# Kernel optimization log

Hardware: AMD Instinct MI355X
Metric: run time of the kernel (lower is better)

Reference implementation:

```python
import jax, jax.numpy as jnp
import numpy as np

B, L, DIM = 1, 2048, 512
DHEAD = 64
HEADS = DIM // DHEAD  # 8
KS = 127              # kernel_size (odd)
EXP = 4


def setup_inputs() -> dict:
    key = jax.random.key(0)
    ks = jax.random.split(key, 8)
    sc = 0.02
    rnd = lambda k, shape: (jax.random.normal(k, shape, jnp.float32) * sc)
    return {
        "x": jax.random.normal(ks[0], (B, L, DIM), jnp.float32),
        "ln1_g": jnp.ones((DIM,), jnp.float32),
        "ln1_b": jnp.zeros((DIM,), jnp.float32),
        "qkv_w": rnd(ks[1], (DIM, 3 * DIM)),
        "qkv_b": jnp.zeros((3 * DIM,), jnp.float32),
        "rpb": rnd(ks[2], (HEADS, 2 * KS - 1)),
        "proj_w": rnd(ks[3], (DIM, DIM)),
        "proj_b": jnp.zeros((DIM,), jnp.float32),
        "ln2_g": jnp.ones((DIM,), jnp.float32),
        "ln2_b": jnp.zeros((DIM,), jnp.float32),
        "ff1_w": rnd(ks[4], (DIM, DIM * EXP)),
        "ff1_b": jnp.zeros((DIM * EXP,), jnp.float32),
        "ff2_w": rnd(ks[5], (DIM * EXP, DIM)),
        "ff2_b": jnp.zeros((DIM,), jnp.float32),
    }


def _layernorm(x, g, b, eps=1e-5):
    m = x.mean(-1, keepdims=True)
    v = ((x - m) ** 2).mean(-1, keepdims=True)
    return (x - m) * jax.lax.rsqrt(v + eps) * g + b


def _neighborhood_attn_1d(x, qkv_w, qkv_b, rpb, proj_w, proj_b):
    # NATTEN NeighborhoodAttention1D: window of KS keys per query, clamped
    # at sequence edges so every query sees exactly KS keys (requires L >= KS).
    b, l, dim = x.shape
    qkv = (x @ qkv_w + qkv_b).reshape(b, l, 3, HEADS, DHEAD)
    q, k, v = qkv[:, :, 0], qkv[:, :, 1], qkv[:, :, 2]  # [b,l,h,d]
    scale = DHEAD ** -0.5
    # window start per query, clamped to stay in-bounds
    starts = jnp.clip(jnp.arange(l) - KS // 2, 0, l - KS)          # [l]
    idx = starts[:, None] + jnp.arange(KS)                         # [l,KS]
    kg = k[:, idx]                                                 # [b,l,KS,h,d]
    vg = v[:, idx]                                                 # [b,l,KS,h,d]
    logits = jnp.einsum('blhd,blkhd->blhk', q * scale, kg)         # [b,l,h,KS]
    # relative-position bias: index = (j - i) + (KS - 1), in [0, 2KS-2]
    bias_idx = idx - jnp.arange(l)[:, None] + (KS - 1)             # [l,KS]
    logits = logits + rpb[:, bias_idx].transpose(1, 0, 2)[None]    # [1,l,h,KS]
    attn = jax.nn.softmax(logits, axis=-1)
    out = jnp.einsum('blhk,blkhd->blhd', attn, vg).reshape(b, l, dim)
    return out @ proj_w + proj_b


def reference(x, ln1_g, ln1_b, qkv_w, qkv_b, rpb, proj_w, proj_b,
              ln2_g, ln2_b, ff1_w, ff1_b, ff2_w, ff2_b):
    x = x + _neighborhood_attn_1d(_layernorm(x, ln1_g, ln1_b),
                                  qkv_w, qkv_b, rpb, proj_w, proj_b)
    h = _layernorm(x, ln2_g, ln2_b)
    h = jax.nn.gelu(h @ ff1_w + ff1_b, approximate=False) @ ff2_w + ff2_b
    return x + h
```

## Files before the change

kernel.cpp:

```cpp
#include <hip/hip_runtime.h>
#include <hip/hip_bf16.h>

static constexpr int Lc     = 2048;
static constexpr int DIMc   = 512;
static constexpr int HEADSc = 8;
static constexpr int DHEADc = 64;
static constexpr int KSc    = 127;
static constexpr int NQKVc  = 1536;

typedef __attribute__((ext_vector_type(8))) short short8;
typedef __attribute__((ext_vector_type(4))) float f32x4;
typedef unsigned short u16;
typedef unsigned int u32;

__device__ __forceinline__ float b2f(u16 s) {
  return __uint_as_float(((u32)s) << 16);
}
__device__ __forceinline__ u16 f2b(float x) {
  u32 u = __float_as_uint(x);
  return (u16)((u + 0x7fffu + ((u >> 16) & 1u)) >> 16);
}
__device__ __forceinline__ void gload16(const void* g, void* l) {
  __builtin_amdgcn_global_load_lds(
      (const __attribute__((address_space(1))) u32*)g,
      (__attribute__((address_space(3))) u32*)l, 16, 0, 0);
}

__global__ __launch_bounds__(256) void prep_kernel(
    const float* __restrict__ w0, const float* __restrict__ w1,
    const float* __restrict__ w2, const float* __restrict__ w3,
    u16* __restrict__ o0, u16* __restrict__ o1, u16* __restrict__ o2,
    u16* __restrict__ o3, const float* __restrict__ xin,
    const float* __restrict__ g, const float* __restrict__ b,
    u16* __restrict__ lnout) {
  __shared__ float tl[32][33];
  __shared__ float rs[4], rq[4], stat[2];
  const int tid = threadIdx.x;
  if (blockIdx.x >= 3072) {
    const int row = blockIdx.x - 3072;
    const float* rp = xin + (size_t)row * DIMc;
    float v0 = rp[tid];
    float v1 = rp[tid + 256];
    float s = v0 + v1;
    float sq = v0 * v0 + v1 * v1;
#pragma unroll
    for (int o = 32; o > 0; o >>= 1) {
      s += __shfl_down(s, o);
      sq += __shfl_down(sq, o);
    }
    const int wid = tid >> 6, lane = tid & 63;
    if (lane == 0) { rs[wid] = s; rq[wid] = sq; }
    __syncthreads();
    if (tid == 0) {
      float S = rs[0] + rs[1] + rs[2] + rs[3];
      float Q = rq[0] + rq[1] + rq[2] + rq[3];
      float m = S / DIMc;
      float var = Q / DIMc - m * m;
      stat[0] = m;
      stat[1] = rsqrtf(var + 1e-5f);
    }
    __syncthreads();
    const float m = stat[0], r = stat[1];
    lnout[(size_t)row * DIMc + tid] = f2b((v0 - m) * r * g[tid] + b[tid]);
    lnout[(size_t)row * DIMc + tid + 256] =
        f2b((v1 - m) * r * g[tid + 256] + b[tid + 256]);
    return;
  }
  int t = blockIdx.x;
  const float* W;
  u16* O;
  int K, N;
  if (t < 768)       { W = w0; O = o0; K = 512;  N = 1536; }
  else if (t < 1024) { W = w1; O = o1; K = 512;  N = 512;  t -= 768; }
  else if (t < 2048) { W = w2; O = o2; K = 512;  N = 2048; t -= 1024; }
  else               { W = w3; O = o3; K = 2048; N = 512;  t -= 2048; }
  const int nt = N >> 5;
  const int by = t / nt, bx = t % nt;
  const int c4 = tid & 7, r = tid >> 3;
  {
    const f32x4 v =
        *(const f32x4*)(W + (size_t)(by * 32 + r) * N + bx * 32 + c4 * 4);
    tl[r][c4 * 4 + 0] = v[0];
    tl[r][c4 * 4 + 1] = v[1];
    tl[r][c4 * 4 + 2] = v[2];
    tl[r][c4 * 4 + 3] = v[3];
  }
  __syncthreads();
  {
    ushort4 pk = {f2b(tl[c4 * 4 + 0][r]), f2b(tl[c4 * 4 + 1][r]),
                  f2b(tl[c4 * 4 + 2][r]), f2b(tl[c4 * 4 + 3][r])};
    *(ushort4*)(O + (size_t)(bx * 32 + r) * K + by * 32 + c4 * 4) = pk;
  }
}

__global__ __launch_bounds__(256) void ln2_kernel(const float* __restrict__ in,
                                                  const float* __restrict__ g,
                                                  const float* __restrict__ b,
                                                  u16* __restrict__ out) {
  const int row = blockIdx.x;
  const int tid = threadIdx.x;
  const float* rp = in + (size_t)row * DIMc;
  float v0 = rp[tid];
  float v1 = rp[tid + 256];
  float s = v0 + v1;
  float sq = v0 * v0 + v1 * v1;
  __shared__ float rs[4], rq[4], stat[2];
#pragma unroll
  for (int o = 32; o > 0; o >>= 1) {
    s += __shfl_down(s, o);
    sq += __shfl_down(sq, o);
  }
  const int wid = tid >> 6, lane = tid & 63;
  if (lane == 0) { rs[wid] = s; rq[wid] = sq; }
  __syncthreads();
  if (tid == 0) {
    float S = rs[0] + rs[1] + rs[2] + rs[3];
    float Q = rq[0] + rq[1] + rq[2] + rq[3];
    float m = S / DIMc;
    float var = Q / DIMc - m * m;
    stat[0] = m;
    stat[1] = rsqrtf(var + 1e-5f);
  }
  __syncthreads();
  const float m = stat[0], r = stat[1];
  out[(size_t)row * DIMc + tid] = f2b((v0 - m) * r * g[tid] + b[tid]);
  out[(size_t)row * DIMc + tid + 256] =
      f2b((v1 - m) * r * g[tid + 256] + b[tid + 256]);
}

template <int OP, typename OUT_T>
__global__ __launch_bounds__(128) void mfma_gemm(
    const u16* __restrict__ A, const u16* __restrict__ Bt,
    const float* __restrict__ bias, const float* __restrict__ res,
    OUT_T* __restrict__ C, int M, int N, int K) {
  constexpr int BK = 64;
  __shared__ __align__(16) u16 As[2][64 * BK];
  __shared__ __align__(16) u16 Bs[2][64 * BK];
  const int tid = threadIdx.x;
  const int wave = tid >> 6, lane = tid & 63;
  const int m0 = blockIdx.y * 64, n0 = blockIdx.x * 64;
  const int wn = wave * 32;
  const int T = K / BK;

  f32x4 acc[4][2] = {};

  const int fr = lane & 15;
  const int hi = lane >> 4;

  const int lrow = wave * 8 + (lane >> 3);
  const int lcol = ((lane & 7) ^ (lane >> 3)) * 8;

#define STAGE(k0, buf)                                                        \
  {                                                                           \
    _Pragma("unroll") for (int p = 0; p < 4; ++p) {                           \
      gload16(A + (size_t)(m0 + p * 16 + lrow) * K + (k0) + lcol,             \
              &As[buf][p * 1024 + wave * 512]);                               \
      gload16(Bt + (size_t)(n0 + p * 16 + lrow) * K + (k0) + lcol,            \
              &Bs[buf][p * 1024 + wave * 512]);                               \
    }                                                                         \
  }

  STAGE(0, 0);
  STAGE(BK, 1);

  for (int t = 0; t < T; ++t) {
    const int cur = t & 1;
    if (t + 1 < T) {
      asm volatile("s_waitcnt vmcnt(8)" ::: "memory");
    } else {
      asm volatile("s_waitcnt vmcnt(0)" ::: "memory");
    }
    __builtin_amdgcn_s_barrier();

    short8 af[4][2], bf[2][2];
#pragma unroll
    for (int i = 0; i < 4; ++i) {
      const int row = i * 16 + fr;
      const char* rb = (const char*)As[cur] + row * 128;
#pragma unroll
      for (int ks = 0; ks < 2; ++ks)
        af[i][ks] =
            *(const short8*)(rb + ((ks * 64 + hi * 16) ^ ((fr & 7) << 4)));
    }
#pragma unroll
    for (int j = 0; j < 2; ++j) {
      const int row = wn + j * 16 + fr;
      const char* rb = (const char*)Bs[cur] + row * 128;
#pragma unroll
      for (int ks = 0; ks < 2; ++ks)
        bf[j][ks] =
            *(const short8*)(rb + ((ks * 64 + hi * 16) ^ ((fr & 7) << 4)));
    }
    asm volatile("s_waitcnt lgkmcnt(0)" ::: "memory");
    __builtin_amdgcn_sched_barrier(0);
    __builtin_amdgcn_s_barrier();

    if (t + 2 < T) STAGE((t + 2) * BK, cur);

#pragma unroll
    for (int ks = 0; ks < 2; ++ks)
#pragma unroll
      for (int i = 0; i < 4; ++i)
#pragma unroll
        for (int j = 0; j < 2; ++j)
          acc[i][j] = __builtin_amdgcn_mfma_f32_16x16x32_bf16(
              af[i][ks], bf[j][ks], acc[i][j], 0, 0, 0);
  }
#undef STAGE

  const int cl = lane & 15;
  const int rbase = (lane >> 4) * 4;
#pragma unroll
  for (int i = 0; i < 4; ++i) {
#pragma unroll
    for (int j = 0; j < 2; ++j) {
      const int c = n0 + wn + j * 16 + cl;
      const float bv = bias[c];
#pragma unroll
      for (int r = 0; r < 4; ++r) {
        const int row = m0 + i * 16 + rbase + r;
        float v = acc[i][j][r] + bv;
        if (OP == 1) v = 0.5f * v * (1.0f + erff(v * 0.70710678118f));
        ((u16*)C)[(size_t)row * N + c] = f2b(v);
      }
    }
  }
}

__global__ __launch_bounds__(256, 1) void mfma_gemm_ks(
    const u16* __restrict__ A, const u16* __restrict__ Bt,
    const float* __restrict__ bias, const float* __restrict__ res,
    float* __restrict__ C, int M, int N, int K) {
  constexpr int BK = 32;
  __shared__ __align__(16) char LB[65536];
  const int tid = threadIdx.x;
  const int wave = tid >> 6, lane = tid & 63;
  const int m0 = blockIdx.y * 64, n0 = blockIdx.x * 64;
  const int kslice = K >> 2;
  const int kbeg = wave * kslice;
  const int T = kslice / BK;
  char* myb = LB + wave * 16384;

  f32x4 acc[4][4] = {};
  const int fr = lane & 15;
  const int hi = lane >> 4;

  const int lrow = lane >> 2;
  const int lcol = ((lane & 3) ^ ((lane >> 2) & 3)) * 8;

#define KSTAGE(k0, b)                                                         \
  {                                                                           \
    _Pragma("unroll") for (int p = 0; p < 4; ++p) {                           \
      gload16(A + (size_t)(m0 + p * 16 + lrow) * K + (k0) + lcol,             \
              myb + (b) * 8192 + p * 1024);                                   \
      gload16(Bt + (size_t)(n0 + p * 16 + lrow) * K + (k0) + lcol,            \
              myb + (b) * 8192 + 4096 + p * 1024);                            \
    }                                                                         \
  }

  KSTAGE(kbeg, 0);
  KSTAGE(kbeg + BK, 1);

  for (int t = 0; t < T; ++t) {
    const int cur = t & 1;
    if (t + 1 < T) {
      asm volatile("s_waitcnt vmcnt(8)" ::: "memory");
    } else {
      asm volatile("s_waitcnt vmcnt(0)" ::: "memory");
    }

    short8 af[4], bf[4];
#pragma unroll
    for (int i = 0; i < 4; ++i) {
      const char* rb = myb + cur * 8192 + (i * 16 + fr) * 64;
      af[i] = *(const short8*)(rb + ((hi * 16) ^ ((fr & 3) << 4)));
    }
#pragma unroll
    for (int j = 0; j < 4; ++j) {
      const char* rb = myb + cur * 8192 + 4096 + (j * 16 + fr) * 64;
      bf[j] = *(const short8*)(rb + ((hi * 16) ^ ((fr & 3) << 4)));
    }
    asm volatile("s_waitcnt lgkmcnt(0)" ::: "memory");
    __builtin_amdgcn_sched_barrier(0);

    if (t + 2 < T) KSTAGE(kbeg + (t + 2) * BK, cur);

    __builtin_amdgcn_s_setprio(1);
#pragma unroll
    for (int i = 0; i < 4; ++i)
#pragma unroll
      for (int j = 0; j < 4; ++j)
        acc[i][j] = __builtin_amdgcn_mfma_f32_16x16x32_bf16(af[i], bf[j],
                                                            acc[i][j], 0, 0, 0);
    __builtin_amdgcn_s_setprio(0);
  }
#undef KSTAGE

  __syncthreads();
  float* red = (float*)LB;
  const int rbase = hi * 4;
#pragma unroll
  for (int i = 0; i < 4; ++i)
#pragma unroll
    for (int j = 0; j < 4; ++j)
#pragma unroll
      for (int r = 0; r < 4; ++r)
        red[wave * 4096 + (i * 16 + rbase + r) * 64 + j * 16 + fr] =
            acc[i][j][r];
  __syncthreads();
#pragma unroll
  for (int q = 0; q < 4; ++q) {
    const int idx = q * 1024 + tid * 4;
    const int row = idx >> 6, col = idx & 63;
    f32x4 s = *(const f32x4*)&red[idx];
#pragma unroll
    for (int w = 1; w < 4; ++w) s += *(const f32x4*)&red[w * 4096 + idx];
    const f32x4 bb = *(const f32x4*)&bias[n0 + col];
    const size_t o = (size_t)(m0 + row) * N + n0 + col;
    const f32x4 rr = *(const f32x4*)&res[o];
    s += bb + rr;
    *(f32x4*)&C[o] = s;
  }
}

__global__ __launch_bounds__(256) void attn_mfma(const u16* __restrict__ qkv,
                                                 const float* __restrict__ rpb,
                                                 u16* __restrict__ out) {
  constexpr int NR = 192, NT = 12, PP = 200;
  __shared__ __align__(16) u16 Ks[NR * DHEADc];
  __shared__ __align__(16) u16 Vt[DHEADc * NR];
  __shared__ __align__(16) u16 Ps[4][16 * PP];
  __shared__ float rp[2 * KSc - 1];
  const int h = blockIdx.y, l0 = blockIdx.x * 64, tid = threadIdx.x;
  const int wv = tid >> 6, lane = tid & 63;
  const int fr = lane & 15, hi = lane >> 4;

  int s_min = l0 - 63;
  if (s_min < 0) s_min = 0;
  if (s_min > Lc - KSc) s_min = Lc - KSc;

  for (int i = tid; i < 2 * KSc - 1; i += 256) rp[i] = rpb[h * (2 * KSc - 1) + i];

#pragma unroll
  for (int rd = 0; rd < 6; ++rd) {
    const int linear = rd * 4096 + wv * 1024 + lane * 16;
    const int row = linear >> 7;
    const int seg = (linear >> 4) & 7;
    const int segp = seg ^ (row & 7);
    int gl = s_min + row;
    if (gl > Lc - 1) gl = Lc - 1;
    gload16(qkv + (size_t)gl * NQKVc + DIMc + h * DHEADc + segp * 8,
            (char*)Ks + rd * 4096 + wv * 1024);
  }

#pragma unroll
  for (int rd = 0; rd < 3; ++rd) {
    const int t = rd * 256 + tid;
    const int rpair = t >> 3, seg = t & 7;
    const int r0 = rpair * 2;
    int g0 = s_min + r0, g1 = s_min + r0 + 1;
    if (g0 > Lc - 1) g0 = Lc - 1;
    if (g1 > Lc - 1) g1 = Lc - 1;
    const short8 a =
        *(const short8*)(qkv + (size_t)g0 * NQKVc + 2 * DIMc + h * DHEADc + seg * 8);
    const short8 bq =
        *(const short8*)(qkv + (size_t)g1 * NQKVc + 2 * DIMc + h * DHEADc + seg * 8);
#pragma unroll
    for (int j = 0; j < 8; ++j) {
      const int d = seg * 8 + j;
      int byte = d * (NR * 2) + r0 * 2;
      byte ^= (d & 7) << 4;
      *(u32*)((char*)Vt + byte) =
          ((u32)(u16)a[j]) | (((u32)(u16)bq[j]) << 16);
    }
  }

  const int lq = l0 + wv * 16 + fr;
  short8 qf[2];
#pragma unroll
  for (int ks = 0; ks < 2; ++ks)
    qf[ks] = *(const short8*)(qkv + (size_t)lq * NQKVc + h * DHEADc + ks * 32 + hi * 8);

  __syncthreads();

  f32x4 S[NT] = {};
  __builtin_amdgcn_s_setprio(1);
#pragma unroll
  for (int jt = 0; jt < NT; ++jt) {
#pragma unroll
    for (int ks = 0; ks < 2; ++ks) {
      int byte = (jt * 16 + fr) * 128 + ks * 64 + hi * 16;
      byte ^= (fr & 7) << 4;
      const short8 kf = *(const short8*)((const char*)Ks + byte);
      S[jt] = __builtin_amdgcn_mfma_f32_16x16x32_bf16(qf[ks], kf, S[jt], 0, 0, 0);
    }
  }
  __builtin_amdgcn_s_setprio(0);

  float inv4[4];
#pragma unroll
  for (int r = 0; r < 4; ++r) {
    const int l = l0 + wv * 16 + hi * 4 + r;
    int st = l - 63;
    if (st < 0) st = 0;
    if (st > Lc - KSc) st = Lc - KSc;
    float mx = -3e38f;
#pragma unroll
    for (int jt = 0; jt < NT; ++jt) {
      const int pos = s_min + jt * 16 + fr;
      const int j = pos - st;
      float v = -3e38f;
      if (j >= 0 && j <= KSc - 1) v = S[jt][r] * 0.125f + rp[pos - l + KSc - 1];
      S[jt][r] = v;
      mx = fmaxf(mx, v);
    }
#pragma unroll
    for (int o = 1; o < 16; o <<= 1) mx = fmaxf(mx, __shfl_xor(mx, o));
    float sum = 0.f;
#pragma unroll
    for (int jt = 0; jt < NT; ++jt) {
      const float e = __expf(S[jt][r] - mx);
      S[jt][r] = e;
      sum += e;
    }
#pragma unroll
    for (int o = 1; o < 16; o <<= 1) sum += __shfl_xor(sum, o);
    inv4[r] = 1.f / sum;
  }

#pragma unroll
  for (int jt = 0; jt < NT; ++jt)
#pragma unroll
    for (int r = 0; r < 4; ++r)
      Ps[wv][(hi * 4 + r) * PP + jt * 16 + fr] = f2b(S[jt][r] * inv4[r]);

  f32x4 O[4] = {};
  __builtin_amdgcn_s_setprio(1);
#pragma unroll
  for (int ks = 0; ks < 6; ++ks) {
    const short8 pa =
        *(const short8*)((const char*)Ps[wv] + fr * (PP * 2) + ks * 64 + hi * 16);
#pragma unroll
    for (int dt = 0; dt < 4; ++dt) {
      int byte = (dt * 16 + fr) * (NR * 2) + ks * 64 + hi * 16;
      byte ^= (fr & 7) << 4;
      const short8 vb = *(const short8*)((const char*)Vt + byte);
      O[dt] = __builtin_amdgcn_mfma_f32_16x16x32_bf16(pa, vb, O[dt], 0, 0, 0);
    }
  }
  __builtin_amdgcn_s_setprio(0);

#pragma unroll
  for (int dt = 0; dt < 4; ++dt)
#pragma unroll
    for (int r = 0; r < 4; ++r)
      out[(size_t)(l0 + wv * 16 + hi * 4 + r) * DIMc + h * DHEADc + dt * 16 + fr] =
          f2b(O[dt][r]);
}

extern "C" void kernel_launch(void* const* d_in, const int* in_sizes, int n_in,
                              void* d_out, int out_size, void* d_ws,
                              size_t ws_size, hipStream_t stream) {
  const float* x      = (const float*)d_in[0];
  const float* ln1_g  = (const float*)d_in[1];
  const float* ln1_b  = (const float*)d_in[2];
  const float* qkv_w  = (const float*)d_in[3];
  const float* qkv_b  = (const float*)d_in[4];
  const float* rpb    = (const float*)d_in[5];
  const float* proj_w = (const float*)d_in[6];
  const float* proj_b = (const float*)d_in[7];
  const float* ln2_g  = (const float*)d_in[8];
  const float* ln2_b  = (const float*)d_in[9];
  const float* ff1_w  = (const float*)d_in[10];
  const float* ff1_b  = (const float*)d_in[11];
  const float* ff2_w  = (const float*)d_in[12];
  const float* ff2_b  = (const float*)d_in[13];
  float* out = (float*)d_out;

  char* ws = (char*)d_ws;
  u16*   lnbuf   = (u16*)(ws);
  u16*   qkvbuf  = (u16*)(ws + ((size_t)2  << 20));
  u16*   attnbuf = (u16*)(ws + ((size_t)8  << 20));
  float* x2      = (float*)(ws + ((size_t)10 << 20));
  u16*   ff1buf  = (u16*)(ws + ((size_t)14 << 20));
  u16*   wt_qkv  = (u16*)(ws + ((size_t)22 << 20));
  u16*   wt_proj = (u16*)(ws + ((size_t)23 << 20) + ((size_t)512 << 10));
  u16*   wt_ff1  = (u16*)(ws + ((size_t)24 << 20));
  u16*   wt_ff2  = (u16*)(ws + ((size_t)26 << 20));

  prep_kernel<<<5120, 256, 0, stream>>>(qkv_w, proj_w, ff1_w, ff2_w, wt_qkv,
                                        wt_proj, wt_ff1, wt_ff2, x, ln1_g,
                                        ln1_b, lnbuf);
  mfma_gemm<0, u16><<<dim3(NQKVc / 64, Lc / 64), 128, 0, stream>>>(
      lnbuf, wt_qkv, qkv_b, nullptr, qkvbuf, Lc, NQKVc, DIMc);
  attn_mfma<<<dim3(Lc / 64, HEADSc), 256, 0, stream>>>(qkvbuf, rpb, attnbuf);
  mfma_gemm_ks<<<dim3(DIMc / 64, Lc / 64), 256, 0, stream>>>(
      attnbuf, wt_proj, proj_b, x, x2, Lc, DIMc, DIMc);
  ln2_kernel<<<Lc, 256, 0, stream>>>(x2, ln2_g, ln2_b, lnbuf);
  mfma_gemm<1, u16><<<dim3(4 * DIMc / 64, Lc / 64), 128, 0, stream>>>(
      lnbuf, wt_ff1, ff1_b, nullptr, ff1buf, Lc, 4 * DIMc, DIMc);
  mfma_gemm_ks<<<dim3(DIMc / 64, Lc / 64), 256, 0, stream>>>(
      ff1buf, wt_ff2, ff2_b, x2, out, Lc, DIMc, 4 * DIMc);
}
```

Before: 67.15 us.

## Fuse proj, LN2, FF1 and FF2 into one persistent kernel with grid barriers

```diff
diff --git a/kernel.cpp b/kernel.cpp
--- a/kernel.cpp
+++ b/kernel.cpp
@@ -32,10 +32,11 @@
     u16* __restrict__ o0, u16* __restrict__ o1, u16* __restrict__ o2,
     u16* __restrict__ o3, const float* __restrict__ xin,
     const float* __restrict__ g, const float* __restrict__ b,
-    u16* __restrict__ lnout) {
+    u16* __restrict__ lnout, u32* __restrict__ bar) {
   __shared__ float tl[32][33];
   __shared__ float rs[4], rq[4], stat[2];
   const int tid = threadIdx.x;
+  if (blockIdx.x == 0 && tid < 8) bar[tid] = 0;
   if (blockIdx.x >= 3072) {
     const int row = blockIdx.x - 3072;
     const float* rp = xin + (size_t)row * DIMc;
@@ -93,46 +94,10 @@
   }
 }
 
-__global__ __launch_bounds__(256) void ln2_kernel(const float* __restrict__ in,
-                                                  const float* __restrict__ g,
-                                                  const float* __restrict__ b,
-                                                  u16* __restrict__ out) {
-  const int row = blockIdx.x;
-  const int tid = threadIdx.x;
-  const float* rp = in + (size_t)row * DIMc;
-  float v0 = rp[tid];
-  float v1 = rp[tid + 256];
-  float s = v0 + v1;
-  float sq = v0 * v0 + v1 * v1;
-  __shared__ float rs[4], rq[4], stat[2];
-#pragma unroll
-  for (int o = 32; o > 0; o >>= 1) {
-    s += __shfl_down(s, o);
-    sq += __shfl_down(sq, o);
-  }
-  const int wid = tid >> 6, lane = tid & 63;
-  if (lane == 0) { rs[wid] = s; rq[wid] = sq; }
-  __syncthreads();
-  if (tid == 0) {
-    float S = rs[0] + rs[1] + rs[2] + rs[3];
-    float Q = rq[0] + rq[1] + rq[2] + rq[3];
-    float m = S / DIMc;
-    float var = Q / DIMc - m * m;
-    stat[0] = m;
-    stat[1] = rsqrtf(var + 1e-5f);
-  }
-  __syncthreads();
-  const float m = stat[0], r = stat[1];
-  out[(size_t)row * DIMc + tid] = f2b((v0 - m) * r * g[tid] + b[tid]);
-  out[(size_t)row * DIMc + tid + 256] =
-      f2b((v1 - m) * r * g[tid + 256] + b[tid + 256]);
-}
-
-template <int OP, typename OUT_T>
 __global__ __launch_bounds__(128) void mfma_gemm(
     const u16* __restrict__ A, const u16* __restrict__ Bt,
-    const float* __restrict__ bias, const float* __restrict__ res,
-    OUT_T* __restrict__ C, int M, int N, int K) {
+    const float* __restrict__ bias, u16* __restrict__ C, int M, int N,
+    int K) {
   constexpr int BK = 64;
   __shared__ __align__(16) u16 As[2][64 * BK];
   __shared__ __align__(16) u16 Bs[2][64 * BK];
@@ -143,10 +108,8 @@
   const int T = K / BK;
 
   f32x4 acc[4][2] = {};
-
   const int fr = lane & 15;
   const int hi = lane >> 4;
-
   const int lrow = wave * 8 + (lane >> 3);
   const int lcol = ((lane & 7) ^ (lane >> 3)) * 8;
 
@@ -219,107 +182,9 @@
 #pragma unroll
       for (int r = 0; r < 4; ++r) {
         const int row = m0 + i * 16 + rbase + r;
-        float v = acc[i][j][r] + bv;
-        if (OP == 1) v = 0.5f * v * (1.0f + erff(v * 0.70710678118f));
-        ((u16*)C)[(size_t)row * N + c] = f2b(v);
+        C[(size_t)row * N + c] = f2b(acc[i][j][r] + bv);
       }
     }
-  }
-}
-
-__global__ __launch_bounds__(256, 1) void mfma_gemm_ks(
-    const u16* __restrict__ A, const u16* __restrict__ Bt,
-    const float* __restrict__ bias, const float* __restrict__ res,
-    float* __restrict__ C, int M, int N, int K) {
-  constexpr int BK = 32;
-  __shared__ __align__(16) char LB[65536];
-  const int tid = threadIdx.x;
-  const int wave = tid >> 6, lane = tid & 63;
-  const int m0 = blockIdx.y * 64, n0 = blockIdx.x * 64;
-  const int kslice = K >> 2;
-  const int kbeg = wave * kslice;
-  const int T = kslice / BK;
-  char* myb = LB + wave * 16384;
-
-  f32x4 acc[4][4] = {};
-  const int fr = lane & 15;
-  const int hi = lane >> 4;
-
-  const int lrow = lane >> 2;
-  const int lcol = ((lane & 3) ^ ((lane >> 2) & 3)) * 8;
-
-#define KSTAGE(k0, b)                                                         \
-  {                                                                           \
-    _Pragma("unroll") for (int p = 0; p < 4; ++p) {                           \
-      gload16(A + (size_t)(m0 + p * 16 + lrow) * K + (k0) + lcol,             \
-              myb + (b) * 8192 + p * 1024);                                   \
-      gload16(Bt + (size_t)(n0 + p * 16 + lrow) * K + (k0) + lcol,            \
-              myb + (b) * 8192 + 4096 + p * 1024);                            \
-    }                                                                         \
-  }
-
-  KSTAGE(kbeg, 0);
-  KSTAGE(kbeg + BK, 1);
-
-  for (int t = 0; t < T; ++t) {
-    const int cur = t & 1;
-    if (t + 1 < T) {
-      asm volatile("s_waitcnt vmcnt(8)" ::: "memory");
-    } else {
-      asm volatile("s_waitcnt vmcnt(0)" ::: "memory");
-    }
-
-    short8 af[4], bf[4];
-#pragma unroll
-    for (int i = 0; i < 4; ++i) {
-      const char* rb = myb + cur * 8192 + (i * 16 + fr) * 64;
-      af[i] = *(const short8*)(rb + ((hi * 16) ^ ((fr & 3) << 4)));
-    }
-#pragma unroll
-    for (int j = 0; j < 4; ++j) {
-      const char* rb = myb + cur * 8192 + 4096 + (j * 16 + fr) * 64;
-      bf[j] = *(const short8*)(rb + ((hi * 16) ^ ((fr & 3) << 4)));
-    }
-    asm volatile("s_waitcnt lgkmcnt(0)" ::: "memory");
-    __builtin_amdgcn_sched_barrier(0);
-
-    if (t + 2 < T) KSTAGE(kbeg + (t + 2) * BK, cur);
-
-    __builtin_amdgcn_s_setprio(1);
-#pragma unroll
-    for (int i = 0; i < 4; ++i)
-#pragma unroll
-      for (int j = 0; j < 4; ++j)
-        acc[i][j] = __builtin_amdgcn_mfma_f32_16x16x32_bf16(af[i], bf[j],
-                                                            acc[i][j], 0, 0, 0);
-    __builtin_amdgcn_s_setprio(0);
-  }
-#undef KSTAGE
-
-  __syncthreads();
-  float* red = (float*)LB;
-  const int rbase = hi * 4;
-#pragma unroll
-  for (int i = 0; i < 4; ++i)
-#pragma unroll
-    for (int j = 0; j < 4; ++j)
-#pragma unroll
-      for (int r = 0; r < 4; ++r)
-        red[wave * 4096 + (i * 16 + rbase + r) * 64 + j * 16 + fr] =
-            acc[i][j][r];
-  __syncthreads();
-#pragma unroll
-  for (int q = 0; q < 4; ++q) {
-    const int idx = q * 1024 + tid * 4;
-    const int row = idx >> 6, col = idx & 63;
-    f32x4 s = *(const f32x4*)&red[idx];
-#pragma unroll
-    for (int w = 1; w < 4; ++w) s += *(const f32x4*)&red[w * 4096 + idx];
-    const f32x4 bb = *(const f32x4*)&bias[n0 + col];
-    const size_t o = (size_t)(m0 + row) * N + n0 + col;
-    const f32x4 rr = *(const f32x4*)&res[o];
-    s += bb + rr;
-    *(f32x4*)&C[o] = s;
   }
 }
 
@@ -456,6 +321,250 @@
     for (int r = 0; r < 4; ++r)
       out[(size_t)(l0 + wv * 16 + hi * 4 + r) * DIMc + h * DHEADc + dt * 16 + fr] =
           f2b(O[dt][r]);
+}
+
+__device__ __forceinline__ void gridbar(u32* c, int tid) {
+  __threadfence();
+  __syncthreads();
+  if (tid == 0) {
+    u32 old = __hip_atomic_fetch_add(c, 1, __ATOMIC_ACQ_REL,
+                                     __HIP_MEMORY_SCOPE_AGENT);
+    u32 target = (old / 256u + 1u) * 256u;
+    while (__hip_atomic_load(c, __ATOMIC_ACQUIRE, __HIP_MEMORY_SCOPE_AGENT) <
+           target) {
+      __builtin_amdgcn_s_sleep(8);
+    }
+  }
+  __syncthreads();
+  __threadfence();
+}
+
+__global__ __launch_bounds__(256, 1) void tail_kernel(
+    const u16* __restrict__ attnbuf, const u16* __restrict__ wt_proj,
+    const float* __restrict__ proj_b, const float* __restrict__ x,
+    float* __restrict__ x2, const float* __restrict__ ln2_g,
+    const float* __restrict__ ln2_b, u16* __restrict__ lnbuf,
+    const u16* __restrict__ wt_ff1, const float* __restrict__ ff1_b,
+    u16* __restrict__ ff1buf, const u16* __restrict__ wt_ff2,
+    const float* __restrict__ ff2_b, float* __restrict__ outp,
+    u32* __restrict__ bar) {
+  __shared__ __align__(16) char LB[65536];
+  const int tid = threadIdx.x;
+  const int wave = tid >> 6, lane = tid & 63;
+  const int fr = lane & 15;
+  const int hi = lane >> 4;
+  const int blk = blockIdx.x;
+
+#define KS_GEMM(Ap, Bp, Kv, biasp, resp, Cp, Nv)                              \
+  {                                                                           \
+    constexpr int BK = 32;                                                    \
+    const int m0 = (blk >> 3) * 64, n0 = (blk & 7) * 64;                      \
+    const int kslice = (Kv) >> 2;                                             \
+    const int kbeg = wave * kslice;                                           \
+    const int T = kslice / BK;                                                \
+    char* myb = LB + wave * 16384;                                            \
+    f32x4 acc[4][4] = {};                                                     \
+    const int lrow = lane >> 2;                                               \
+    const int lcol = ((lane & 3) ^ ((lane >> 2) & 3)) * 8;                    \
+    for (int s = 0; s < 2; ++s) {                                             \
+      _Pragma("unroll") for (int p = 0; p < 4; ++p) {                         \
+        gload16((Ap) + (size_t)(m0 + p * 16 + lrow) * (Kv) + kbeg + s * BK +  \
+                    lcol,                                                     \
+                myb + s * 8192 + p * 1024);                                   \
+        gload16((Bp) + (size_t)(n0 + p * 16 + lrow) * (Kv) + kbeg + s * BK +  \
+                    lcol,                                                     \
+                myb + s * 8192 + 4096 + p * 1024);                            \
+      }                                                                       \
+    }                                                                         \
+    for (int t = 0; t < T; ++t) {                                             \
+      const int cur = t & 1;                                                  \
+      if (t + 1 < T) {                                                        \
+        asm volatile("s_waitcnt vmcnt(8)" ::: "memory");                      \
+      } else {                                                                \
+        asm volatile("s_waitcnt vmcnt(0)" ::: "memory");                      \
+      }                                                                       \
+      short8 af[4], bf[4];                                                    \
+      _Pragma("unroll") for (int i = 0; i < 4; ++i) {                         \
+        const char* rb = myb + cur * 8192 + (i * 16 + fr) * 64;               \
+        af[i] = *(const short8*)(rb + ((hi * 16) ^ ((fr & 3) << 4)));         \
+      }                                                                       \
+      _Pragma("unroll") for (int j = 0; j < 4; ++j) {                         \
+        const char* rb = myb + cur * 8192 + 4096 + (j * 16 + fr) * 64;        \
+        bf[j] = *(const short8*)(rb + ((hi * 16) ^ ((fr & 3) << 4)));         \
+      }                                                                       \
+      asm volatile("s_waitcnt lgkmcnt(0)" ::: "memory");                      \
+      __builtin_amdgcn_sched_barrier(0);                                      \
+      if (t + 2 < T) {                                                        \
+        _Pragma("unroll") for (int p = 0; p < 4; ++p) {                       \
+          gload16((Ap) + (size_t)(m0 + p * 16 + lrow) * (Kv) + kbeg +         \
+                      (t + 2) * BK + lcol,                                    \
+                  myb + cur * 8192 + p * 1024);                               \
+          gload16((Bp) + (size_t)(n0 + p * 16 + lrow) * (Kv) + kbeg +         \
+                      (t + 2) * BK + lcol,                                    \
+                  myb + cur * 8192 + 4096 + p * 1024);                        \
+        }                                                                     \
+      }                                                                       \
+      __builtin_amdgcn_s_setprio(1);                                          \
+      _Pragma("unroll") for (int i = 0; i < 4; ++i)                           \
+          _Pragma("unroll") for (int j = 0; j < 4; ++j) acc[i][j] =           \
+          __builtin_amdgcn_mfma_f32_16x16x32_bf16(af[i], bf[j], acc[i][j],    \
+                                                  0, 0, 0);                   \
+      __builtin_amdgcn_s_setprio(0);                                          \
+    }                                                                         \
+    __syncthreads();                                                          \
+    float* red = (float*)LB;                                                  \
+    const int rbase = hi * 4;                                                 \
+    _Pragma("unroll") for (int i = 0; i < 4; ++i)                             \
+        _Pragma("unroll") for (int j = 0; j < 4; ++j)                         \
+        _Pragma("unroll") for (int r = 0; r < 4; ++r)                         \
+        red[wave * 4096 + (i * 16 + rbase + r) * 64 + j * 16 + fr] =          \
+        acc[i][j][r];                                                         \
+    __syncthreads();                                                          \
+    _Pragma("unroll") for (int q = 0; q < 4; ++q) {                           \
+      const int idx = q * 1024 + tid * 4;                                     \
+      const int row = idx >> 6, col = idx & 63;                               \
+      f32x4 s = *(const f32x4*)&red[idx];                                     \
+      _Pragma("unroll") for (int w = 1; w < 4; ++w) s +=                      \
+          *(const f32x4*)&red[w * 4096 + idx];                                \
+      const f32x4 bb = *(const f32x4*)&(biasp)[n0 + col];                     \
+      const size_t o = (size_t)(m0 + row) * (Nv) + n0 + col;                  \
+      const f32x4 rr = *(const f32x4*)&(resp)[o];                             \
+      s += bb + rr;                                                           \
+      *(f32x4*)&(Cp)[o] = s;                                                  \
+    }                                                                         \
+  }
+
+  KS_GEMM(attnbuf, wt_proj, DIMc, proj_b, x, x2, DIMc);
+  gridbar(bar + 0, tid);
+
+  {
+    __shared__ float rs[4], rq[4], stat[2];
+    for (int rr = 0; rr < 8; ++rr) {
+      const int row = blk * 8 + rr;
+      const size_t base = (size_t)row * DIMc;
+      const float v0 = x2[base + tid];
+      const float v1 = x2[base + tid + 256];
+      float s = v0 + v1;
+      float sq = v0 * v0 + v1 * v1;
+#pragma unroll
+      for (int o = 32; o > 0; o >>= 1) {
+        s += __shfl_down(s, o);
+        sq += __shfl_down(sq, o);
+      }
+      if (lane == 0) { rs[wave] = s; rq[wave] = sq; }
+      __syncthreads();
+      if (tid == 0) {
+        float S = rs[0] + rs[1] + rs[2] + rs[3];
+        float Q = rq[0] + rq[1] + rq[2] + rq[3];
+        float m = S / DIMc;
+        float var = Q / DIMc - m * m;
+        stat[0] = m;
+        stat[1] = rsqrtf(var + 1e-5f);
+      }
+      __syncthreads();
+      const float m = stat[0], r = stat[1];
+      lnbuf[base + tid] = f2b((v0 - m) * r * ln2_g[tid] + ln2_b[tid]);
+      lnbuf[base + tid + 256] =
+          f2b((v1 - m) * r * ln2_g[tid + 256] + ln2_b[tid + 256]);
+      __syncthreads();
+    }
+  }
+  gridbar(bar + 1, tid);
+
+  {
+    constexpr int BK = 64, K = DIMc, N = 4 * DIMc;
+    const int grp = wave >> 1;
+    const int gw = wave & 1;
+    u16* As = (u16*)(LB + grp * 32768);
+    u16* Bs = (u16*)(LB + grp * 32768 + 16384);
+    const int wn = gw * 32;
+    const int lrow = gw * 8 + (lane >> 3);
+    const int lcol = ((lane & 7) ^ (lane >> 3)) * 8;
+    const int T = K / BK;
+
+    for (int rep = 0; rep < 2; ++rep) {
+      const int tile = blk * 4 + grp * 2 + rep;
+      const int n0 = (tile & 31) * 64, m0 = (tile >> 5) * 64;
+      f32x4 acc[4][2] = {};
+
+#define F1STAGE(k0, buf)                                                      \
+  {                                                                           \
+    _Pragma("unroll") for (int p = 0; p < 4; ++p) {                           \
+      gload16(lnbuf + (size_t)(m0 + p * 16 + lrow) * K + (k0) + lcol,         \
+              &As[(buf) * 4096 + p * 1024 + gw * 512]);                       \
+      gload16(wt_ff1 + (size_t)(n0 + p * 16 + lrow) * K + (k0) + lcol,        \
+              &Bs[(buf) * 4096 + p * 1024 + gw * 512]);                       \
+    }                                                                         \
+  }
+      F1STAGE(0, 0);
+      F1STAGE(BK, 1);
+      for (int t = 0; t < T; ++t) {
+        const int cur = t & 1;
+        if (t + 1 < T) {
+          asm volatile("s_waitcnt vmcnt(8)" ::: "memory");
+        } else {
+          asm volatile("s_waitcnt vmcnt(0)" ::: "memory");
+        }
+        __builtin_amdgcn_s_barrier();
+
+        short8 af[4][2], bf[2][2];
+#pragma unroll
+        for (int i = 0; i < 4; ++i) {
+          const char* rb = (const char*)&As[cur * 4096] + (i * 16 + fr) * 128;
+#pragma unroll
+          for (int ks = 0; ks < 2; ++ks)
+            af[i][ks] =
+                *(const short8*)(rb + ((ks * 64 + hi * 16) ^ ((fr & 7) << 4)));
+        }
+#pragma unroll
+        for (int j = 0; j < 2; ++j) {
+          const char* rb =
+              (const char*)&Bs[cur * 4096] + (wn + j * 16 + fr) * 128;
+#pragma unroll
+          for (int ks = 0; ks < 2; ++ks)
+            bf[j][ks] =
+                *(const short8*)(rb + ((ks * 64 + hi * 16) ^ ((fr & 7) << 4)));
+        }
+        asm volatile("s_waitcnt lgkmcnt(0)" ::: "memory");
+        __builtin_amdgcn_sched_barrier(0);
+        __builtin_amdgcn_s_barrier();
+
+        if (t + 2 < T) F1STAGE((t + 2) * BK, cur);
+
+#pragma unroll
+        for (int ks = 0; ks < 2; ++ks)
+#pragma unroll
+          for (int i = 0; i < 4; ++i)
+#pragma unroll
+            for (int j = 0; j < 2; ++j)
+              acc[i][j] = __builtin_amdgcn_mfma_f32_16x16x32_bf16(
+                  af[i][ks], bf[j][ks], acc[i][j], 0, 0, 0);
+      }
+#undef F1STAGE
+
+      const int cl = lane & 15;
+      const int rbase = (lane >> 4) * 4;
+#pragma unroll
+      for (int i = 0; i < 4; ++i) {
+#pragma unroll
+        for (int j = 0; j < 2; ++j) {
+          const int c = n0 + wn + j * 16 + cl;
+          const float bv = ff1_b[c];
+#pragma unroll
+          for (int r = 0; r < 4; ++r) {
+            const int row = m0 + i * 16 + rbase + r;
+            float v = acc[i][j][r] + bv;
+            v = 0.5f * v * (1.0f + erff(v * 0.70710678118f));
+            ff1buf[(size_t)row * N + c] = f2b(v);
+          }
+        }
+      }
+    }
+  }
+  gridbar(bar + 2, tid);
+
+  KS_GEMM(ff1buf, wt_ff2, 4 * DIMc, ff2_b, x2, outp, DIMc);
+#undef KS_GEMM
 }
 
 extern "C" void kernel_launch(void* const* d_in, const int* in_sizes, int n_in,
@@ -487,18 +596,15 @@
   u16*   wt_proj = (u16*)(ws + ((size_t)23 << 20) + ((size_t)512 << 10));
   u16*   wt_ff1  = (u16*)(ws + ((size_t)24 << 20));
   u16*   wt_ff2  = (u16*)(ws + ((size_t)26 << 20));
+  u32*   bar     = (u32*)(ws + ((size_t)30 << 20));
 
   prep_kernel<<<5120, 256, 0, stream>>>(qkv_w, proj_w, ff1_w, ff2_w, wt_qkv,
                                         wt_proj, wt_ff1, wt_ff2, x, ln1_g,
-                                        ln1_b, lnbuf);
-  mfma_gemm<0, u16><<<dim3(NQKVc / 64, Lc / 64), 128, 0, stream>>>(
-      lnbuf, wt_qkv, qkv_b, nullptr, qkvbuf, Lc, NQKVc, DIMc);
+                                        ln1_b, lnbuf, bar);
+  mfma_gemm<<<dim3(NQKVc / 64, Lc / 64), 128, 0, stream>>>(
+      lnbuf, wt_qkv, qkv_b, qkvbuf, Lc, NQKVc, DIMc);
   attn_mfma<<<dim3(Lc / 64, HEADSc), 256, 0, stream>>>(qkvbuf, rpb, attnbuf);
-  mfma_gemm_ks<<<dim3(DIMc / 64, Lc / 64), 256, 0, stream>>>(
-      attnbuf, wt_proj, proj_b, x, x2, Lc, DIMc, DIMc);
-  ln2_kernel<<<Lc, 256, 0, stream>>>(x2, ln2_g, ln2_b, lnbuf);
-  mfma_gemm<1, u16><<<dim3(4 * DIMc / 64, Lc / 64), 128, 0, stream>>>(
-      lnbuf, wt_ff1, ff1_b, nullptr, ff1buf, Lc, 4 * DIMc, DIMc);
-  mfma_gemm_ks<<<dim3(DIMc / 64, Lc / 64), 256, 0, stream>>>(
-      ff1buf, wt_ff2, ff2_b, x2, out, Lc, DIMc, 4 * DIMc);
-}
+  tail_kernel<<<256, 256, 0, stream>>>(attnbuf, wt_proj, proj_b, x, x2, ln2_g,
+                                       ln2_b, lnbuf, wt_ff1, ff1_b, ff1buf,
+                                       wt_ff2, ff2_b, out, bar);
+}
```

After: 221.1 us. 3.29x slower.

## Fuse LayerNorm2 into projection GEMM epilogue via per-row-block atomic counter

Applied to the files above, without the earlier changes.

```diff
diff --git a/kernel.cpp b/kernel.cpp
--- a/kernel.cpp
+++ b/kernel.cpp
@@ -32,10 +32,11 @@
     u16* __restrict__ o0, u16* __restrict__ o1, u16* __restrict__ o2,
     u16* __restrict__ o3, const float* __restrict__ xin,
     const float* __restrict__ g, const float* __restrict__ b,
-    u16* __restrict__ lnout) {
+    u16* __restrict__ lnout, u32* __restrict__ bar) {
   __shared__ float tl[32][33];
   __shared__ float rs[4], rq[4], stat[2];
   const int tid = threadIdx.x;
+  if (blockIdx.x == 0 && tid < 32) bar[tid] = 0;
   if (blockIdx.x >= 3072) {
     const int row = blockIdx.x - 3072;
     const float* rp = xin + (size_t)row * DIMc;
@@ -93,41 +94,6 @@
   }
 }
 
-__global__ __launch_bounds__(256) void ln2_kernel(const float* __restrict__ in,
-                                                  const float* __restrict__ g,
-                                                  const float* __restrict__ b,
-                                                  u16* __restrict__ out) {
-  const int row = blockIdx.x;
-  const int tid = threadIdx.x;
-  const float* rp = in + (size_t)row * DIMc;
-  float v0 = rp[tid];
-  float v1 = rp[tid + 256];
-  float s = v0 + v1;
-  float sq = v0 * v0 + v1 * v1;
-  __shared__ float rs[4], rq[4], stat[2];
-#pragma unroll
-  for (int o = 32; o > 0; o >>= 1) {
-    s += __shfl_down(s, o);
-    sq += __shfl_down(sq, o);
-  }
-  const int wid = tid >> 6, lane = tid & 63;
-  if (lane == 0) { rs[wid] = s; rq[wid] = sq; }
-  __syncthreads();
-  if (tid == 0) {
-    float S = rs[0] + rs[1] + rs[2] + rs[3];
-    float Q = rq[0] + rq[1] + rq[2] + rq[3];
-    float m = S / DIMc;
-    float var = Q / DIMc - m * m;
-    stat[0] = m;
-    stat[1] = rsqrtf(var + 1e-5f);
-  }
-  __syncthreads();
-  const float m = stat[0], r = stat[1];
-  out[(size_t)row * DIMc + tid] = f2b((v0 - m) * r * g[tid] + b[tid]);
-  out[(size_t)row * DIMc + tid + 256] =
-      f2b((v1 - m) * r * g[tid + 256] + b[tid + 256]);
-}
-
 template <int OP, typename OUT_T>
 __global__ __launch_bounds__(128) void mfma_gemm(
     const u16* __restrict__ A, const u16* __restrict__ Bt,
@@ -227,12 +193,16 @@
   }
 }
 
+template <bool LN2F>
 __global__ __launch_bounds__(256, 1) void mfma_gemm_ks(
     const u16* __restrict__ A, const u16* __restrict__ Bt,
     const float* __restrict__ bias, const float* __restrict__ res,
-    float* __restrict__ C, int M, int N, int K) {
+    float* __restrict__ C, int M, int N, int K,
+    const float* __restrict__ ln_g, const float* __restrict__ ln_b,
+    u16* __restrict__ lnout, u32* __restrict__ bar) {
   constexpr int BK = 32;
   __shared__ __align__(16) char LB[65536];
+  __shared__ u32 oldc;
   const int tid = threadIdx.x;
   const int wave = tid >> 6, lane = tid & 63;
   const int m0 = blockIdx.y * 64, n0 = blockIdx.x * 64;
@@ -320,6 +290,50 @@
     const f32x4 rr = *(const f32x4*)&res[o];
     s += bb + rr;
     *(f32x4*)&C[o] = s;
+  }
+
+  if (LN2F) {
+    __threadfence();
+    __syncthreads();
+    if (tid == 0)
+      oldc = __hip_atomic_fetch_add(&bar[blockIdx.y], 1, __ATOMIC_ACQ_REL,
+                                    __HIP_MEMORY_SCOPE_AGENT);
+    __syncthreads();
+    if (oldc == 7) {
+      __threadfence();
+      const int le = lane * 8;
+      const f32x4 g0 = *(const f32x4*)&ln_g[le];
+      const f32x4 g1 = *(const f32x4*)&ln_g[le + 4];
+      const f32x4 b0 = *(const f32x4*)&ln_b[le];
+      const f32x4 b1 = *(const f32x4*)&ln_b[le + 4];
+#pragma unroll 4
+      for (int it = 0; it < 16; ++it) {
+        const int row = m0 + it * 4 + wave;
+        const size_t base = (size_t)row * DIMc + le;
+        const f32x4 a = *(const f32x4*)&C[base];
+        const f32x4 c = *(const f32x4*)&C[base + 4];
+        float s = a[0] + a[1] + a[2] + a[3] + c[0] + c[1] + c[2] + c[3];
+        float q = a[0] * a[0] + a[1] * a[1] + a[2] * a[2] + a[3] * a[3] +
+                  c[0] * c[0] + c[1] * c[1] + c[2] * c[2] + c[3] * c[3];
+#pragma unroll
+        for (int o = 1; o < 64; o <<= 1) {
+          s += __shfl_xor(s, o);
+          q += __shfl_xor(q, o);
+        }
+        const float mean = s / DIMc;
+        const float rstd = rsqrtf(q / DIMc - mean * mean + 1e-5f);
+        ushort4 p0 = {f2b((a[0] - mean) * rstd * g0[0] + b0[0]),
+                      f2b((a[1] - mean) * rstd * g0[1] + b0[1]),
+                      f2b((a[2] - mean) * rstd * g0[2] + b0[2]),
+                      f2b((a[3] - mean) * rstd * g0[3] + b0[3])};
+        ushort4 p1 = {f2b((c[0] - mean) * rstd * g1[0] + b1[0]),
+                      f2b((c[1] - mean) * rstd * g1[1] + b1[1]),
+                      f2b((c[2] - mean) * rstd * g1[2] + b1[2]),
+                      f2b((c[3] - mean) * rstd * g1[3] + b1[3])};
+        *(ushort4*)&lnout[base] = p0;
+        *(ushort4*)&lnout[base + 4] = p1;
+      }
+    }
   }
 }
 
@@ -487,18 +501,20 @@
   u16*   wt_proj = (u16*)(ws + ((size_t)23 << 20) + ((size_t)512 << 10));
   u16*   wt_ff1  = (u16*)(ws + ((size_t)24 << 20));
   u16*   wt_ff2  = (u16*)(ws + ((size_t)26 << 20));
+  u32*   bar     = (u32*)(ws + ((size_t)30 << 20));
 
   prep_kernel<<<5120, 256, 0, stream>>>(qkv_w, proj_w, ff1_w, ff2_w, wt_qkv,
                                         wt_proj, wt_ff1, wt_ff2, x, ln1_g,
-                                        ln1_b, lnbuf);
+                                        ln1_b, lnbuf, bar);
   mfma_gemm<0, u16><<<dim3(NQKVc / 64, Lc / 64), 128, 0, stream>>>(
       lnbuf, wt_qkv, qkv_b, nullptr, qkvbuf, Lc, NQKVc, DIMc);
   attn_mfma<<<dim3(Lc / 64, HEADSc), 256, 0, stream>>>(qkvbuf, rpb, attnbuf);
-  mfma_gemm_ks<<<dim3(DIMc / 64, Lc / 64), 256, 0, stream>>>(
-      attnbuf, wt_proj, proj_b, x, x2, Lc, DIMc, DIMc);
-  ln2_kernel<<<Lc, 256, 0, stream>>>(x2, ln2_g, ln2_b, lnbuf);
+  mfma_gemm_ks<true><<<dim3(DIMc / 64, Lc / 64), 256, 0, stream>>>(
+      attnbuf, wt_proj, proj_b, x, x2, Lc, DIMc, DIMc, ln2_g, ln2_b, lnbuf,
+      bar);
   mfma_gemm<1, u16><<<dim3(4 * DIMc / 64, Lc / 64), 128, 0, stream>>>(
       lnbuf, wt_ff1, ff1_b, nullptr, ff1buf, Lc, 4 * DIMc, DIMc);
-  mfma_gemm_ks<<<dim3(DIMc / 64, Lc / 64), 256, 0, stream>>>(
-      ff1buf, wt_ff2, ff2_b, x2, out, Lc, DIMc, 4 * DIMc);
-}
+  mfma_gemm_ks<false><<<dim3(DIMc / 64, Lc / 64), 256, 0, stream>>>(
+      ff1buf, wt_ff2, ff2_b, x2, out, Lc, DIMc, 4 * DIMc, nullptr, nullptr,
+      nullptr, nullptr);
+}
```

After: 105.0 us. 1.56x slower.
